# Performance work log

Hardware: AMD Instinct MI355X
Metric: run time of the kernel (lower is better)

The kernel has to match this reference:

```python
import jax, jax.numpy as jnp
import numpy as np

EMBED_DIM = 2048
NUM_HEADS = 32
NUM_KV_HEADS = 8
HEAD_DIM = EMBED_DIM // NUM_HEADS  # 64
Q_PER_KV = NUM_HEADS // NUM_KV_HEADS  # 4
B, S = 4, 1024


def setup_inputs() -> dict:
    key = jax.random.key(0)
    kq, kk, kv = jax.random.split(key, 3)
    query = jax.random.normal(kq, (B, S, EMBED_DIM), dtype=jnp.float32)
    k = jax.random.normal(kk, (B, S, NUM_KV_HEADS * HEAD_DIM), dtype=jnp.float32)
    v = jax.random.normal(kv, (B, S, NUM_KV_HEADS * HEAD_DIM), dtype=jnp.float32)
    return {"query": query, "key": k, "value": v}


def reference(query, key, value):
    b, s, _ = query.shape
    # [b, s, H, d] and [b, s, Hkv, d]
    q = query.reshape(b, s, NUM_HEADS, HEAD_DIM)
    k = key.reshape(b, s, NUM_KV_HEADS, HEAD_DIM)
    v = value.reshape(b, s, NUM_KV_HEADS, HEAD_DIM)
    # expand kv heads: repeat each kv head Q_PER_KV times -> [b, s, H, d]
    k = jnp.repeat(k, Q_PER_KV, axis=2)
    v = jnp.repeat(v, Q_PER_KV, axis=2)
    scale = 1.0 / jnp.sqrt(jnp.float32(HEAD_DIM))
    # scores: [b, H, s_q, s_k]
    scores = jnp.einsum('bqhd,bkhd->bhqk', q, k) * scale
    attn = jax.nn.softmax(scores, axis=-1)
    out = jnp.einsum('bhqk,bkhd->bqhd', attn, v).reshape(b, s, EMBED_DIM)
    return out, attn
```

## Files before the change

### kernel.cpp

```cpp
#include <hip/hip_runtime.h>

#define NB 4
#define SEQ 1024
#define NH 32
#define NKV 8
#define HD 64
#define QBLK 32
#define VSTR 72

typedef __attribute__((ext_vector_type(8))) short short8;
typedef __attribute__((ext_vector_type(4))) float f32x4;
typedef __attribute__((ext_vector_type(4))) unsigned short u16x4;

static __device__ __forceinline__ unsigned short f2bf(float f) {
  union { float f; unsigned u; } x; x.f = f;
  unsigned u = x.u;
  u += 0x7fffu + ((u >> 16) & 1u);
  return (unsigned short)(u >> 16);
}
static __device__ __forceinline__ float bf2f(unsigned short h) {
  union { unsigned u; float f; } x; x.u = ((unsigned)h) << 16;
  return x.f;
}

__global__ __launch_bounds__(512, 4) void gqa_kernel(
    const float* __restrict__ Qg, const float* __restrict__ Kg,
    const float* __restrict__ Vg, float* __restrict__ Og) {
  __shared__ unsigned short Ph[QBLK * 512];
  __shared__ unsigned short VsT[2][HD * VSTR];
  __shared__ float redmax[QBLK][8];
  __shared__ float redsum[QBLK][8];

  const int tid = threadIdx.x;
  const int lane = tid & 63;
  const int wid = tid >> 6;
  const int li = lane & 15;
  const int g = lane >> 4;

  const int hw = blockIdx.x;
  const int gid = (hw & 7) * 512 + (hw >> 3);

  const int qt = gid & 31;
  const int h = (gid >> 5) & 31;
  const int b = gid >> 10;
  const int hkv = h >> 2;
  const int q0 = qt * QBLK;

  const float* Qp = Qg + ((size_t)b * SEQ) * 2048 + h * 64;
  const float* Kp = Kg + ((size_t)b * SEQ) * 512 + hkv * 64;
  const float* Vp = Vg + ((size_t)b * SEQ) * 512 + hkv * 64;
  float* Outp = Og + ((size_t)b * SEQ) * 2048 + h * 64;
  float* Attnp = Og + (size_t)NB * SEQ * 2048
               + (((size_t)(b * NH + h)) * SEQ + q0) * SEQ;

  char* phb = (char*)&Ph[0];

  short8 aq[2][2];
#pragma unroll
  for (int m = 0; m < 2; ++m)
#pragma unroll
    for (int dh = 0; dh < 2; ++dh) {
      const float* qp = Qp + (size_t)(q0 + m * 16 + li) * 2048 + dh * 32 + g * 8;
      float4 x = *(const float4*)qp;
      float4 y = *(const float4*)(qp + 4);
      short8 t;
      t[0] = (short)f2bf(x.x * 0.125f); t[1] = (short)f2bf(x.y * 0.125f);
      t[2] = (short)f2bf(x.z * 0.125f); t[3] = (short)f2bf(x.w * 0.125f);
      t[4] = (short)f2bf(y.x * 0.125f); t[5] = (short)f2bf(y.y * 0.125f);
      t[6] = (short)f2bf(y.z * 0.125f); t[7] = (short)f2bf(y.w * 0.125f);
      aq[m][dh] = t;
    }

  f32x4 acc[2][8];
  f32x4 zero4 = {0.f, 0.f, 0.f, 0.f};
#pragma unroll
  for (int m = 0; m < 2; ++m)
#pragma unroll
    for (int j = 0; j < 8; ++j) acc[m][j] = zero4;

  const int colbase = wid * 128 + li;
#pragma unroll
  for (int j = 0; j < 8; ++j) {
    int col = colbase + j * 16;
    short8 bk[2];
#pragma unroll
    for (int dh = 0; dh < 2; ++dh) {
      const float* kp = Kp + (size_t)col * 512 + dh * 32 + g * 8;
      float4 x = *(const float4*)kp;
      float4 y = *(const float4*)(kp + 4);
      short8 t;
      t[0]=(short)f2bf(x.x); t[1]=(short)f2bf(x.y); t[2]=(short)f2bf(x.z); t[3]=(short)f2bf(x.w);
      t[4]=(short)f2bf(y.x); t[5]=(short)f2bf(y.y); t[6]=(short)f2bf(y.z); t[7]=(short)f2bf(y.w);
      bk[dh] = t;
    }
#pragma unroll
    for (int m = 0; m < 2; ++m) {
      acc[m][j] = __builtin_amdgcn_mfma_f32_16x16x32_bf16(aq[m][0], bk[0], acc[m][j], 0, 0, 0);
      acc[m][j] = __builtin_amdgcn_mfma_f32_16x16x32_bf16(aq[m][1], bk[1], acc[m][j], 0, 0, 0);
    }
  }

#pragma unroll
  for (int m = 0; m < 2; ++m)
#pragma unroll
    for (int r = 0; r < 4; ++r) {
      float mx = -1e30f;
#pragma unroll
      for (int j = 0; j < 8; ++j) mx = fmaxf(mx, acc[m][j][r]);
      mx = fmaxf(mx, __shfl_xor(mx, 1));
      mx = fmaxf(mx, __shfl_xor(mx, 2));
      mx = fmaxf(mx, __shfl_xor(mx, 4));
      mx = fmaxf(mx, __shfl_xor(mx, 8));
      if (li == 0) redmax[m * 16 + g * 4 + r][wid] = mx;
    }
  __syncthreads();

#pragma unroll
  for (int m = 0; m < 2; ++m)
#pragma unroll
    for (int r = 0; r < 4; ++r) {
      int row = m * 16 + g * 4 + r;
      float mx = fmaxf(fmaxf(fmaxf(redmax[row][0], redmax[row][1]),
                             fmaxf(redmax[row][2], redmax[row][3])),
                       fmaxf(fmaxf(redmax[row][4], redmax[row][5]),
                             fmaxf(redmax[row][6], redmax[row][7])));
      float s = 0.f;
#pragma unroll
      for (int j = 0; j < 8; ++j) {
        float e = __expf(acc[m][j][r] - mx);
        acc[m][j][r] = e;
        s += e;
      }
      s += __shfl_xor(s, 1);
      s += __shfl_xor(s, 2);
      s += __shfl_xor(s, 4);
      s += __shfl_xor(s, 8);
      if (li == 0) redsum[row][wid] = s;
    }
  __syncthreads();

#pragma unroll
  for (int m = 0; m < 2; ++m)
#pragma unroll
    for (int r = 0; r < 4; ++r) {
      int row = m * 16 + g * 4 + r;
      float L = 0.f;
#pragma unroll
      for (int w = 0; w < 8; ++w) L += redsum[row][w];
      float inv = 1.0f / L;
#pragma unroll
      for (int j = 0; j < 8; ++j) acc[m][j][r] *= inv;
    }

  const int m_o = wid >> 2;
  const int nb_ = (wid & 3) * 16;
  f32x4 oacc = zero4;

  const int kd = tid & 63;
  const int kg = tid >> 6;

  for (int h2 = 0; h2 < 2; ++h2) {
    if ((wid >> 2) == h2) {
      int cb = (wid & 3) * 128 + li;
#pragma unroll
      for (int m = 0; m < 2; ++m)
#pragma unroll
        for (int r = 0; r < 4; ++r) {
          int row = m * 16 + g * 4 + r;
#pragma unroll
          for (int j = 0; j < 8; ++j) {
            int col = cb + j * 16;
            *(unsigned short*)(phb + (((row << 10) + (col << 1)) ^ ((row & 7) << 4)))
                = f2bf(acc[m][j][r]);
          }
        }
    }
    {
      int cc = h2 * 8;
      const float* vcol = Vp + (size_t)(cc * 64 + kg * 8) * 512 + kd;
      float pv[8];
#pragma unroll
      for (int i = 0; i < 8; ++i) pv[i] = vcol[(size_t)i * 512];
      ushort4 w0, w1;
      w0.x = f2bf(pv[0]); w0.y = f2bf(pv[1]); w0.z = f2bf(pv[2]); w0.w = f2bf(pv[3]);
      w1.x = f2bf(pv[4]); w1.y = f2bf(pv[5]); w1.z = f2bf(pv[6]); w1.w = f2bf(pv[7]);
      *(ushort4*)(&VsT[0][kd * VSTR + kg * 8]) = w0;
      *(ushort4*)(&VsT[0][kd * VSTR + kg * 8 + 4]) = w1;
    }
    __syncthreads();

    {
      int rsub = tid >> 7;
      int c128 = tid & 127;
#pragma unroll
      for (int i = 0; i < 8; ++i) {
        int row = i * 4 + rsub;
        u16x4 u = *(const u16x4*)(phb + (((row << 10) + (c128 << 3)) ^ ((row & 7) << 4)));
        f32x4 f;
        f.x = bf2f(u.x); f.y = bf2f(u.y); f.z = bf2f(u.z); f.w = bf2f(u.w);
        __builtin_nontemporal_store(f, (f32x4*)(Attnp + (size_t)row * SEQ + h2 * 512 + c128 * 4));
      }
    }

    for (int c = 0; c < 8; ++c) {
      float pv[8];
      if (c < 7) {
        int cc = h2 * 8 + c + 1;
        const float* vcol = Vp + (size_t)(cc * 64 + kg * 8) * 512 + kd;
#pragma unroll
        for (int i = 0; i < 8; ++i) pv[i] = vcol[(size_t)i * 512];
      }
      const unsigned short* vbuf = &VsT[c & 1][0];
#pragma unroll
      for (int kt = 0; kt < 2; ++kt) {
        int lcol = c * 64 + kt * 32 + g * 8;
        int prow = m_o * 16 + li;
        short8 pa = *(const short8*)(phb + (((prow << 10) + (lcol << 1)) ^ ((prow & 7) << 4)));
        short8 vbf = *(const short8*)(&vbuf[(nb_ + li) * VSTR + kt * 32 + g * 8]);
        oacc = __builtin_amdgcn_mfma_f32_16x16x32_bf16(pa, vbf, oacc, 0, 0, 0);
      }
      if (c < 7) {
        ushort4 w0, w1;
        w0.x = f2bf(pv[0]); w0.y = f2bf(pv[1]); w0.z = f2bf(pv[2]); w0.w = f2bf(pv[3]);
        w1.x = f2bf(pv[4]); w1.y = f2bf(pv[5]); w1.z = f2bf(pv[6]); w1.w = f2bf(pv[7]);
        unsigned short* dst = &VsT[(c + 1) & 1][kd * VSTR + kg * 8];
        *(ushort4*)(dst) = w0;
        *(ushort4*)(dst + 4) = w1;
      }
      __syncthreads();
    }
  }

#pragma unroll
  for (int r = 0; r < 4; ++r) {
    int row = q0 + m_o * 16 + g * 4 + r;
    __builtin_nontemporal_store(oacc[r], Outp + (size_t)row * 2048 + nb_ + li);
  }
}

extern "C" void kernel_launch(void* const* d_in, const int* in_sizes, int n_in,
                              void* d_out, int out_size, void* d_ws, size_t ws_size,
                              hipStream_t stream) {
  const float* q = (const float*)d_in[0];
  const float* k = (const float*)d_in[1];
  const float* v = (const float*)d_in[2];
  float* o = (float*)d_out;
  dim3 grid(NB * NH * (SEQ / QBLK));
  dim3 block(512);
  hipLaunchKernelGGL(gqa_kernel, grid, block, 0, stream, q, k, v, o);
}
```

Measured before the change: 529.9 us.

## Load V directly from global into MFMA operands, dropping the LDS V staging buffer

The double-buffered LDS transpose of V and its per-chunk barriers are removed. Each lane now gathers its eight strided V elements straight from global memory and converts them to bf16 for the PV MFMA. The output tile is staged through LDS so it can be written with coalesced vector stores, and launch bounds are raised to target more resident blocks. In exchange, V loads become uncoalesced strided scalar reads that each wave repeats, leaning on the cache for reuse.

```diff
diff --git a/kernel.cpp b/kernel.cpp
--- a/kernel.cpp
+++ b/kernel.cpp
@@ -6,7 +6,6 @@
 #define NKV 8
 #define HD 64
 #define QBLK 32
-#define VSTR 72
 
 typedef __attribute__((ext_vector_type(8))) short short8;
 typedef __attribute__((ext_vector_type(4))) float f32x4;
@@ -23,11 +22,10 @@
   return x.f;
 }
 
-__global__ __launch_bounds__(512, 4) void gqa_kernel(
+__global__ __launch_bounds__(512, 6) void gqa_kernel(
     const float* __restrict__ Qg, const float* __restrict__ Kg,
     const float* __restrict__ Vg, float* __restrict__ Og) {
   __shared__ unsigned short Ph[QBLK * 512];
-  __shared__ unsigned short VsT[2][HD * VSTR];
   __shared__ float redmax[QBLK][8];
   __shared__ float redsum[QBLK][8];
 
@@ -156,9 +154,6 @@
   const int nb_ = (wid & 3) * 16;
   f32x4 oacc = zero4;
 
-  const int kd = tid & 63;
-  const int kg = tid >> 6;
-
   for (int h2 = 0; h2 < 2; ++h2) {
     if ((wid >> 2) == h2) {
       int cb = (wid & 3) * 128 + li;
@@ -174,18 +169,6 @@
                 = f2bf(acc[m][j][r]);
           }
         }
-    }
-    {
-      int cc = h2 * 8;
-      const float* vcol = Vp + (size_t)(cc * 64 + kg * 8) * 512 + kd;
-      float pv[8];
-#pragma unroll
-      for (int i = 0; i < 8; ++i) pv[i] = vcol[(size_t)i * 512];
-      ushort4 w0, w1;
-      w0.x = f2bf(pv[0]); w0.y = f2bf(pv[1]); w0.z = f2bf(pv[2]); w0.w = f2bf(pv[3]);
-      w1.x = f2bf(pv[4]); w1.y = f2bf(pv[5]); w1.z = f2bf(pv[6]); w1.w = f2bf(pv[7]);
-      *(ushort4*)(&VsT[0][kd * VSTR + kg * 8]) = w0;
-      *(ushort4*)(&VsT[0][kd * VSTR + kg * 8 + 4]) = w1;
     }
     __syncthreads();
 
@@ -202,39 +185,40 @@
       }
     }
 
-    for (int c = 0; c < 8; ++c) {
-      float pv[8];
-      if (c < 7) {
-        int cc = h2 * 8 + c + 1;
-        const float* vcol = Vp + (size_t)(cc * 64 + kg * 8) * 512 + kd;
-#pragma unroll
-        for (int i = 0; i < 8; ++i) pv[i] = vcol[(size_t)i * 512];
-      }
-      const unsigned short* vbuf = &VsT[c & 1][0];
-#pragma unroll
-      for (int kt = 0; kt < 2; ++kt) {
-        int lcol = c * 64 + kt * 32 + g * 8;
-        int prow = m_o * 16 + li;
-        short8 pa = *(const short8*)(phb + (((prow << 10) + (lcol << 1)) ^ ((prow & 7) << 4)));
-        short8 vbf = *(const short8*)(&vbuf[(nb_ + li) * VSTR + kt * 32 + g * 8]);
-        oacc = __builtin_amdgcn_mfma_f32_16x16x32_bf16(pa, vbf, oacc, 0, 0, 0);
-      }
-      if (c < 7) {
-        ushort4 w0, w1;
-        w0.x = f2bf(pv[0]); w0.y = f2bf(pv[1]); w0.z = f2bf(pv[2]); w0.w = f2bf(pv[3]);
-        w1.x = f2bf(pv[4]); w1.y = f2bf(pv[5]); w1.z = f2bf(pv[6]); w1.w = f2bf(pv[7]);
-        unsigned short* dst = &VsT[(c + 1) & 1][kd * VSTR + kg * 8];
-        *(ushort4*)(dst) = w0;
-        *(ushort4*)(dst + 4) = w1;
-      }
-      __syncthreads();
-    }
+    const int prow = m_o * 16 + li;
+#pragma unroll 4
+    for (int c = 0; c < 16; ++c) {
+      int lcol = c * 32 + g * 8;
+      short8 pa = *(const short8*)(phb + (((prow << 10) + (lcol << 1)) ^ ((prow & 7) << 4)));
+      const float* vp = Vp + (size_t)(h2 * 512 + c * 32 + g * 8) * 512 + nb_ + li;
+      float v0 = vp[0];
+      float v1 = vp[512];
+      float v2 = vp[1024];
+      float v3 = vp[1536];
+      float v4 = vp[2048];
+      float v5 = vp[2560];
+      float v6 = vp[3072];
+      float v7 = vp[3584];
+      short8 vb;
+      vb[0] = (short)f2bf(v0); vb[1] = (short)f2bf(v1);
+      vb[2] = (short)f2bf(v2); vb[3] = (short)f2bf(v3);
+      vb[4] = (short)f2bf(v4); vb[5] = (short)f2bf(v5);
+      vb[6] = (short)f2bf(v6); vb[7] = (short)f2bf(v7);
+      oacc = __builtin_amdgcn_mfma_f32_16x16x32_bf16(pa, vb, oacc, 0, 0, 0);
+    }
+    __syncthreads();
   }
 
-#pragma unroll
-  for (int r = 0; r < 4; ++r) {
-    int row = q0 + m_o * 16 + g * 4 + r;
-    __builtin_nontemporal_store(oacc[r], Outp + (size_t)row * 2048 + nb_ + li);
+  float* Olds = (float*)&Ph[0];
+#pragma unroll
+  for (int r = 0; r < 4; ++r)
+    Olds[(m_o * 16 + g * 4 + r) * 64 + nb_ + li] = oacc[r];
+  __syncthreads();
+  {
+    int row = tid >> 4;
+    int c4 = (tid & 15) * 4;
+    f32x4 f = *(const f32x4*)(&Olds[row * 64 + c4]);
+    __builtin_nontemporal_store(f, (f32x4*)(Outp + (size_t)(q0 + row) * 2048 + c4));
   }
 }
 
```

Measured after the change: 829.2 us. +56.5%, slower.
